# Kernel tuning notes

Measured on AMD Instinct MI355X. Metric: run time of the kernel, lower is better.

## Reference

```python
import jax, jax.numpy as jnp
import numpy as np


def setup_inputs() -> dict:
    key = jax.random.key(0)
    kx, ky = jax.random.split(key)
    B, N, M, D = 4, 4096, 4096, 128
    xd = jax.random.normal(kx, (B, N, D), dtype=jnp.float32)
    yd = jax.random.normal(ky, (B, M, D), dtype=jnp.float32)
    mask = jnp.ones((B, N, M), dtype=jnp.float32)
    return {"xd": xd, "yd": yd, "mask": mask}


def _pairwise_l2(x, y):
    # x: (B, N, D), y: (B, M, D) -> (B, N, M) euclidean distances
    x2 = jnp.sum(x * x, axis=-1)[:, :, None]          # (B, N, 1)
    y2 = jnp.sum(y * y, axis=-1)[:, None, :]          # (B, 1, M)
    xy = jnp.einsum("bnd,bmd->bnm", x, y)             # (B, N, M)
    d2 = jnp.maximum(x2 + y2 - 2.0 * xy, 0.0)
    return jnp.sqrt(d2)


def reference(xd, yd, mask):
    # NNDFMatcher.forward: orientation='x', smallest=True, topk=None
    dists = _pairwise_l2(xd, yd) * mask               # (B, N, M)
    pairs = jnp.argmin(dists, axis=-1)                # (B, N) int
    top_dists = jnp.min(dists, axis=-1)               # (B, N)
    M = mask.shape[-1]
    # one-hot scatter: match_mask[b, n, pairs[b, n]] = 1
    match_mask = (pairs[..., None] == jnp.arange(M)[None, None, :]).astype(mask.dtype)
    return match_mask, pairs, top_dists
```

## Files before the change

kernel.cpp:

```cpp
#include <hip/hip_runtime.h>


typedef float  f32x4  __attribute__((ext_vector_type(4)));
typedef short  bf16x8 __attribute__((ext_vector_type(8)));

#define PS ((size_t)2097152)

#define WAITVM_(N) asm volatile("s_waitcnt vmcnt(" #N ")" ::: "memory")
#define WAITVM(N)  WAITVM_(N)
#define BAR        __builtin_amdgcn_s_barrier()

__device__ __forceinline__ unsigned short f2bf(float x) {
    unsigned u = __float_as_uint(x);
    u += 0x7FFFu + ((u >> 16) & 1u);
    return (unsigned short)(u >> 16);
}
__device__ __forceinline__ float bf2f(unsigned short s) {
    return __uint_as_float(((unsigned)s) << 16);
}
__device__ __forceinline__ void gload_lds16(const void* g, void* l) {
    __builtin_amdgcn_global_load_lds(
        (const __attribute__((address_space(1))) void*)g,
        (__attribute__((address_space(3))) void*)l, 16, 0, 0);
}

__global__ __launch_bounds__(256) void k_prep(const float* __restrict__ xd,
                                              const float* __restrict__ yd,
                                              unsigned short* __restrict__ pl,
                                              float* __restrict__ ws) {
    __shared__ float sm[4][16];
    int bid  = blockIdx.x;
    int i    = bid >> 10;
    int b    = (bid >> 8) & 3;
    int rblk = bid & 255;
    int tid  = threadIdx.x;
    int kb   = tid >> 6;
    int l    = tid & 63;
    int r    = rblk * 16 + (l & 15);
    int k0   = kb * 32 + ((l >> 4) & 3) * 8;
    const float* src = (i ? yd : xd) + ((size_t)(b * 4096 + r) * 128 + k0);
    float v[8];
    *reinterpret_cast<float4*>(v)     = *reinterpret_cast<const float4*>(src);
    *reinterpret_cast<float4*>(v + 4) = *reinterpret_cast<const float4*>(src + 4);
    bf16x8 hv, mv, lv;
    float s = 0.f;
    #pragma unroll
    for (int e = 0; e < 8; ++e) {
        float x = v[e];
        s = fmaf(x, x, s);
        unsigned short h  = f2bf(x);
        float r1 = x - bf2f(h);
        unsigned short m  = f2bf(r1);
        float r2 = r1 - bf2f(m);
        unsigned short lo = f2bf(r2);
        hv[e] = (short)h; mv[e] = (short)m; lv[e] = (short)lo;
    }
    int rt = rblk >> 3, rb = rblk & 7, kh = kb >> 1, kc = kb & 1;
    size_t base = ((((size_t)((b * 2 + kh) * 32 + rt)) * 8 + rb) * 2 + kc) * 512 + (size_t)l * 8;
    unsigned short* dst = pl + (size_t)(i * 3) * PS;
    *reinterpret_cast<bf16x8*>(dst + base)          = hv;
    *reinterpret_cast<bf16x8*>(dst + base + PS)     = mv;
    *reinterpret_cast<bf16x8*>(dst + base + 2 * PS) = lv;
    s += __shfl_xor(s, 16);
    s += __shfl_xor(s, 32);
    if (l < 16) sm[kb][l] = s;
    __syncthreads();
    if (tid < 16) {
        float t = sm[0][tid] + sm[1][tid] + sm[2][tid] + sm[3][tid];
        ws[(i ? 16384 : 0) + b * 4096 + rblk * 16 + tid] = t;
    }
}

__global__ __launch_bounds__(512, 2) void k_gemm(const float* __restrict__ mask,
                                                 const float* __restrict__ ws,
                                                 const unsigned short* __restrict__ pl,
                                                 float* __restrict__ out,
                                                 float* __restrict__ pv,
                                                 int* __restrict__ pi) {
    __shared__ __align__(16) unsigned short Ab[2][3][8192];
    __shared__ __align__(16) unsigned short Bs[3][8192];
    __shared__ __align__(16) float y2s[2048];
    __shared__ float candv[128][4];
    __shared__ int   candi[128][4];

    const int bid = blockIdx.x;
    const int xcd = bid & 7;
    const int b   = xcd >> 1;
    const int ch  = xcd & 1;
    const int rt  = bid >> 3;
    const int tid = threadIdx.x;
    const int w   = tid >> 6, l = tid & 63;
    const int wr  = w >> 2, wc = w & 3;
    const int lg4 = (l >> 4) & 3, l15 = l & 15;
    const int g0  = b * 4096 + rt * 128;

    float x2r[16];
    #pragma unroll
    for (int mi = 0; mi < 4; ++mi)
        #pragma unroll
        for (int rg = 0; rg < 4; ++rg)
            x2r[mi * 4 + rg] = ws[g0 + wr * 64 + mi * 16 + lg4 * 4 + rg];

    #pragma unroll
    for (int c = 0; c < 6; ++c) {
        const int kh = c / 3, ap = c % 3;
        const unsigned short* Ac = pl + (size_t)ap * PS
            + (((size_t)((b * 2 + kh) * 32 + rt)) << 13);
        const char* g = (const char*)Ac + w * 1024 + l * 16;
        char* dd = (char*)(&Ab[kh][ap][0]) + w * 1024;
        gload_lds16(g, dd);
        gload_lds16(g + 8192, dd + 8192);
    }
    {
        const char* g = (const char*)(ws + 16384 + b * 4096 + ch * 2048) + w * 1024 + l * 16;
        gload_lds16(g, (char*)y2s + w * 1024);
    }

#define STAGE_B(NTT, CC, SLOT) do {                                               \
    const int kh_ = (CC) / 3, bp_ = (CC) % 3;                                     \
    const unsigned short* Bc_ = pl + (size_t)(3 + bp_) * PS                       \
        + (((size_t)((b * 2 + kh_) * 32 + (ch * 16 + (NTT)))) << 13);             \
    const char* g_ = (const char*)Bc_ + w * 1024 + l * 16;                        \
    char* d_ = (char*)(&Bs[SLOT][0]) + w * 1024;                                  \
    gload_lds16(g_, d_);                                                          \
    gload_lds16(g_ + 8192, d_ + 8192);                                            \
} while (0)

    STAGE_B(0, 0, 0);
    STAGE_B(0, 1, 1);
    WAITVM(2);
    BAR;

    float bv[16];
    int   bi[16];
    #pragma unroll
    for (int q = 0; q < 16; ++q) { bv[q] = 3.4e38f; bi[q] = 0; }

    f32x4 acc[4][2];
    float pm[32];

#define MLOAD(K) do {                                                             \
    const int mi_ = (K) >> 3, rg_ = ((K) >> 1) & 3, ni_ = (K) & 1;                \
    pm[K] = mask[(size_t)(g0 + wr * 64 + mi_ * 16 + lg4 * 4 + rg_) * 4096         \
                 + (ch * 2048 + nt * 128 + wc * 32 + ni_ * 16 + l15)];            \
} while (0)

#define ZST(I) do {                                                               \
    const f32x4 z_ = (f32x4){0.f, 0.f, 0.f, 0.f};                                 \
    const int r_ = (tid >> 5) * 8 + (I);                                          \
    *reinterpret_cast<f32x4*>(out + (size_t)(g0 + r_) * 4096                      \
        + ch * 2048 + nt * 128 + ((tid & 31) << 2)) = z_;                         \
} while (0)

#define COMPUTE(CC, SLOT) do {                                                    \
    const int kh_ = (CC) / 3, bp_ = (CC) % 3;                                     \
    const int lim_ = (bp_ == 0) ? 2 : (bp_ == 1) ? 1 : 0;                         \
    bf16x8 bfr_[2][2];                                                            \
    _Pragma("unroll") for (int ni = 0; ni < 2; ++ni)                              \
    _Pragma("unroll") for (int kc = 0; kc < 2; ++kc)                              \
        bfr_[ni][kc] = *reinterpret_cast<const bf16x8*>(                          \
            &Bs[SLOT][(((wc * 2 + ni) * 2 + kc) << 9) + l * 8]);                  \
    __builtin_amdgcn_s_setprio(1);                                                \
    _Pragma("unroll") for (int ap = 0; ap < 3; ++ap) {                            \
        if (ap <= lim_) {                                                         \
            _Pragma("unroll") for (int mi = 0; mi < 4; ++mi) {                    \
                _Pragma("unroll") for (int kc = 0; kc < 2; ++kc) {                \
                    bf16x8 af_ = *reinterpret_cast<const bf16x8*>(                \
                        &Ab[kh_][ap][(((wr * 4 + mi) * 2 + kc) << 9) + l * 8]);   \
                    _Pragma("unroll") for (int ni = 0; ni < 2; ++ni)              \
                        acc[mi][ni] = __builtin_amdgcn_mfma_f32_16x16x32_bf16(    \
                            af_, bfr_[ni][kc], acc[mi][ni], 0, 0, 0);             \
                }                                                                 \
            }                                                                     \
        }                                                                         \
    }                                                                             \
    __builtin_amdgcn_s_setprio(0);                                                \
} while (0)

    for (int nt = 0; nt < 16; ++nt) {
        const int ntn = (nt < 15) ? nt + 1 : 15;
        #pragma unroll
        for (int mi = 0; mi < 4; ++mi)
            #pragma unroll
            for (int ni = 0; ni < 2; ++ni) acc[mi][ni] = (f32x4){0.f, 0.f, 0.f, 0.f};

        STAGE_B(nt, 2, 2);
        MLOAD(0); MLOAD(1); MLOAD(2); MLOAD(3); MLOAD(4); MLOAD(5);
        ZST(0); ZST(1);
        COMPUTE(0, 0);
        WAITVM(10); BAR;
        STAGE_B(nt, 3, 0);
        MLOAD(6); MLOAD(7); MLOAD(8); MLOAD(9); MLOAD(10); MLOAD(11);
        ZST(2); ZST(3);
        COMPUTE(1, 1);
        WAITVM(18); BAR;
        STAGE_B(nt, 4, 1);
        MLOAD(12); MLOAD(13); MLOAD(14); MLOAD(15); MLOAD(16); MLOAD(17);
        ZST(4);
        COMPUTE(2, 2);
        WAITVM(17); BAR;
        STAGE_B(nt, 5, 2);
        MLOAD(18); MLOAD(19); MLOAD(20); MLOAD(21); MLOAD(22); MLOAD(23);
        ZST(5);
        COMPUTE(3, 0);
        WAITVM(16); BAR;
        STAGE_B(ntn, 0, 0);
        MLOAD(24); MLOAD(25); MLOAD(26); MLOAD(27);
        ZST(6);
        COMPUTE(4, 1);
        WAITVM(14); BAR;
        MLOAD(28); MLOAD(29); MLOAD(30); MLOAD(31);
        STAGE_B(ntn, 1, 1);
        ZST(7);
        COMPUTE(5, 2);
        WAITVM(12); BAR;

        WAITVM(3);
        #pragma unroll
        for (int ni = 0; ni < 2; ++ni) {
            const int c = ch * 2048 + nt * 128 + wc * 32 + ni * 16 + l15;
            float y2v = y2s[nt * 128 + wc * 32 + ni * 16 + l15];
            #pragma unroll
            for (int mi = 0; mi < 4; ++mi) {
                #pragma unroll
                for (int rg = 0; rg < 4; ++rg) {
                    float d2 = x2r[mi * 4 + rg] + y2v - 2.0f * acc[mi][ni][rg];
                    float d  = sqrtf(fmaxf(d2, 0.0f)) * pm[mi * 8 + rg * 2 + ni];
                    const int q = mi * 4 + rg;
                    if (d < bv[q]) { bv[q] = d; bi[q] = c; }
                }
            }
        }
    }
#undef STAGE_B
#undef MLOAD
#undef ZST
#undef COMPUTE

    #pragma unroll
    for (int off = 1; off < 16; off <<= 1) {
        #pragma unroll
        for (int q = 0; q < 16; ++q) {
            float ov = __shfl_xor(bv[q], off);
            int   oi = __shfl_xor(bi[q], off);
            if (ov < bv[q] || (ov == bv[q] && oi < bi[q])) { bv[q] = ov; bi[q] = oi; }
        }
    }
    if (l15 == 0) {
        #pragma unroll
        for (int mi = 0; mi < 4; ++mi)
            #pragma unroll
            for (int rg = 0; rg < 4; ++rg) {
                int rowl = wr * 64 + mi * 16 + lg4 * 4 + rg;
                candv[rowl][wc] = bv[mi * 4 + rg];
                candi[rowl][wc] = bi[mi * 4 + rg];
            }
    }
    __syncthreads();
    if (tid < 128) {
        float v  = candv[tid][0];
        int   ix = candi[tid][0];
        #pragma unroll
        for (int t = 1; t < 4; ++t) {
            float v2 = candv[tid][t];
            int   i2 = candi[tid][t];
            if (v2 < v || (v2 == v && i2 < ix)) { v = v2; ix = i2; }
        }
        int grow = g0 + tid;
        pv[grow * 2 + ch] = v;
        pi[grow * 2 + ch] = ix;
    }
}

__global__ __launch_bounds__(256) void k_fin(const float* __restrict__ pv,
                                             const int* __restrict__ pi,
                                             float* __restrict__ out) {
    int t = blockIdx.x * 256 + threadIdx.x;
    float v0 = pv[t * 2], v1 = pv[t * 2 + 1];
    int   i0 = pi[t * 2], i1 = pi[t * 2 + 1];
    bool take1 = (v1 < v0) || (v1 == v0 && i1 < i0);
    float v  = take1 ? v1 : v0;
    int   ix = take1 ? i1 : i0;
    out[67108864 + t]         = (float)ix;
    out[67108864 + 16384 + t] = v;
    out[(size_t)t * 4096 + (size_t)ix] = 1.0f;
}

__global__ __launch_bounds__(256) void k_rowsq(const float* __restrict__ xd,
                                               const float* __restrict__ yd,
                                               float* __restrict__ ws) {
    int tid  = threadIdx.x;
    int wid  = tid >> 6, lane = tid & 63;
    int gr   = blockIdx.x * 4 + wid;
    const float* src = (gr < 16384) ? (xd + (size_t)gr * 128)
                                    : (yd + (size_t)(gr - 16384) * 128);
    float2 v = reinterpret_cast<const float2*>(src)[lane];
    float s  = v.x * v.x + v.y * v.y;
    for (int off = 32; off > 0; off >>= 1) s += __shfl_down(s, off);
    if (lane == 0) ws[gr] = s;
}

__global__ __launch_bounds__(256, 1) void k_main_fb(const float* __restrict__ xd,
                                                    const float* __restrict__ yd,
                                                    const float* __restrict__ mask,
                                                    const float* __restrict__ ws,
                                                    float* __restrict__ pvals,
                                                    int* __restrict__ pidx,
                                                    float* __restrict__ mm) {
    __shared__ __align__(16) float Xs[128 * 128];
    __shared__ __align__(16) float Ys[128 * 128];
    const int bid  = blockIdx.x;
    const int mh   = bid & 1;
    const int rb   = (bid >> 1) & 31;
    const int b    = bid >> 6;
    const int tid  = threadIdx.x;
    const int ty   = tid >> 4;
    const int tx   = tid & 15;
    const int row0 = rb * 128;
    const int m0   = mh * 2048;
    {
        const float4 z = make_float4(0.f, 0.f, 0.f, 0.f);
        size_t base = ((size_t)(b * 4096 + row0)) * 4096 + (size_t)m0;
        for (int r = 0; r < 128; ++r) {
            float4* p = reinterpret_cast<float4*>(mm + base + (size_t)r * 4096);
            p[tid] = z; p[tid + 256] = z;
        }
    }
    {
        int lrow = tid >> 5, slot = tid & 31;
        for (int p = 0; p < 16; ++p) {
            int row  = p * 8 + lrow;
            float4 v = reinterpret_cast<const float4*>(
                           xd + ((size_t)(b * 4096 + row0 + row)) * 128)[slot];
            int ss = slot ^ (row & 31);
            *reinterpret_cast<float4*>(&Xs[row * 128 + (ss << 2)]) = v;
        }
    }
    float x2r[8];
    #pragma unroll
    for (int i = 0; i < 8; ++i) x2r[i] = ws[b * 4096 + row0 + ty * 8 + i];
    const float* y2g = ws + 16384 + b * 4096;
    float bv[8]; int bi[8];
    #pragma unroll
    for (int i = 0; i < 8; ++i) { bv[i] = 3.4e38f; bi[i] = 0; }
    __syncthreads();
    for (int tile = 0; tile < 16; ++tile) {
        const int mbase = m0 + tile * 128;
        {
            int lrow = tid >> 5, slot = tid & 31;
            for (int p = 0; p < 16; ++p) {
                int row  = p * 8 + lrow;
                float4 v = reinterpret_cast<const float4*>(
                               yd + ((size_t)(b * 4096 + mbase + row)) * 128)[slot];
                int ss = slot ^ (row & 31);
                *reinterpret_cast<float4*>(&Ys[row * 128 + (ss << 2)]) = v;
            }
        }
        __syncthreads();
        float acc[8][8];
        #pragma unroll
        for (int i = 0; i < 8; ++i)
            #pragma unroll
            for (int jj = 0; jj < 8; ++jj) acc[i][jj] = 0.0f;
        #pragma unroll 4
        for (int ks = 0; ks < 32; ++ks) {
            float4 bf[8];
            #pragma unroll
            for (int jj = 0; jj < 8; ++jj) {
                int c = jj * 16 + tx;
                bf[jj] = *reinterpret_cast<const float4*>(&Ys[c * 128 + ((ks ^ (c & 31)) << 2)]);
            }
            #pragma unroll
            for (int i = 0; i < 8; ++i) {
                int r = ty * 8 + i;
                float4 a = *reinterpret_cast<const float4*>(&Xs[r * 128 + ((ks ^ (r & 31)) << 2)]);
                #pragma unroll
                for (int jj = 0; jj < 8; ++jj) {
                    acc[i][jj] = fmaf(a.x, bf[jj].x, acc[i][jj]);
                    acc[i][jj] = fmaf(a.y, bf[jj].y, acc[i][jj]);
                    acc[i][jj] = fmaf(a.z, bf[jj].z, acc[i][jj]);
                    acc[i][jj] = fmaf(a.w, bf[jj].w, acc[i][jj]);
                }
            }
        }
        float y2v[8];
        #pragma unroll
        for (int jj = 0; jj < 8; ++jj) y2v[jj] = y2g[mbase + jj * 16 + tx];
        #pragma unroll
        for (int i = 0; i < 8; ++i) {
            int r = ty * 8 + i;
            const float* mr = mask + ((size_t)(b * 4096 + row0 + r)) * 4096;
            #pragma unroll
            for (int jj = 0; jj < 8; ++jj) {
                int   m  = mbase + jj * 16 + tx;
                float d2 = x2r[i] + y2v[jj] - 2.0f * acc[i][jj];
                float d  = sqrtf(fmaxf(d2, 0.0f)) * mr[m];
                if (d < bv[i]) { bv[i] = d; bi[i] = m; }
            }
        }
        __syncthreads();
    }
    float* candv = Xs;
    int*   candi = reinterpret_cast<int*>(Xs + 2048);
    #pragma unroll
    for (int i = 0; i < 8; ++i) {
        int r = ty * 8 + i;
        candv[r * 16 + tx] = bv[i];
        candi[r * 16 + tx] = bi[i];
    }
    __syncthreads();
    if (tid < 128) {
        int   r  = tid;
        float v  = candv[r * 16];
        int   ix = candi[r * 16];
        for (int t = 1; t < 16; ++t) {
            float v2 = candv[r * 16 + t];
            int   i2 = candi[r * 16 + t];
            if (v2 < v || (v2 == v && i2 < ix)) { v = v2; ix = i2; }
        }
        int grow = b * 4096 + row0 + r;
        pvals[grow * 2 + mh] = v;
        pidx [grow * 2 + mh] = ix;
    }
}

__global__ __launch_bounds__(256) void k_fin_fb(const float* __restrict__ pvals,
                                                const int* __restrict__ pidx,
                                                float* __restrict__ out) {
    int t = blockIdx.x * 256 + threadIdx.x;
    float v0 = pvals[t * 2], v1 = pvals[t * 2 + 1];
    int   i0 = pidx [t * 2], i1 = pidx [t * 2 + 1];
    bool take1 = (v1 < v0) || (v1 == v0 && i1 < i0);
    float v  = take1 ? v1 : v0;
    int   ix = take1 ? i1 : i0;
    out[67108864 + t]         = (float)ix;
    out[67108864 + 16384 + t] = v;
    out[(size_t)t * 4096 + (size_t)ix] = 1.0f;
}

extern "C" void kernel_launch(void* const* d_in, const int* in_sizes, int n_in,
                              void* d_out, int out_size, void* d_ws, size_t ws_size,
                              hipStream_t stream) {
    const float* xd   = (const float*)d_in[0];
    const float* yd   = (const float*)d_in[1];
    const float* mask = (const float*)d_in[2];
    float* out = (float*)d_out;
    float* wsf = (float*)d_ws;

    const size_t need = 131072 + 6 * PS * 2 + 262144;
    if (ws_size >= need) {
        unsigned short* pl = (unsigned short*)((char*)d_ws + 131072);
        float* pv = (float*)((char*)d_ws + 131072 + 6 * PS * 2);
        int*   pi = (int*)  ((char*)d_ws + 131072 + 6 * PS * 2 + 131072);
        k_prep <<<2048, 256, 0, stream>>>(xd, yd, pl, wsf);
        k_gemm <<<256,  512, 0, stream>>>(mask, wsf, pl, out, pv, pi);
        k_fin  <<<64,   256, 0, stream>>>(pv, pi, out);
    } else {
        float* pvals = wsf + 32768;
        int*   pidx  = (int*)(wsf + 65536);
        k_rowsq  <<<8192, 256, 0, stream>>>(xd, yd, wsf);
        k_main_fb<<<256,  256, 0, stream>>>(xd, yd, mask, wsf, pvals, pidx, out);
        k_fin_fb <<<64,   256, 0, stream>>>(pvals, pidx, out);
    }
}
```

Baseline: 202.1 us.

## Halve GEMM block tile and stream B fragments through registers instead of LDS

The fused distance/argmin GEMM kernel moves from 512-thread blocks covering 128 rows to 256-thread blocks covering 64 rows, and launches twice as many blocks. B operand fragments are now read straight from global memory into double-buffered registers, one k-chunk ahead, instead of being staged in an LDS ring. This removes the per-chunk barriers and vmcnt bookkeeping, and all mask loads are issued up front each column tile. In exchange each B tile is fetched by twice as many blocks, adding L2/global traffic. Global-load latency is also less hidden, because vmcnt waits for the register prefetch are in-order with the mask loads and zero-stores.

```diff
diff --git a/kernel.cpp b/kernel.cpp
--- a/kernel.cpp
+++ b/kernel.cpp
@@ -6,9 +6,8 @@
 
 #define PS ((size_t)2097152)
 
-#define WAITVM_(N) asm volatile("s_waitcnt vmcnt(" #N ")" ::: "memory")
-#define WAITVM(N)  WAITVM_(N)
-#define BAR        __builtin_amdgcn_s_barrier()
+#define WAITVM0 asm volatile("s_waitcnt vmcnt(0)" ::: "memory")
+#define BAR     __builtin_amdgcn_s_barrier()
 
 __device__ __forceinline__ unsigned short f2bf(float x) {
     unsigned u = __float_as_uint(x);
@@ -71,17 +70,16 @@
     }
 }
 
-__global__ __launch_bounds__(512, 2) void k_gemm(const float* __restrict__ mask,
+__global__ __launch_bounds__(256, 2) void k_gemm(const float* __restrict__ mask,
                                                  const float* __restrict__ ws,
                                                  const unsigned short* __restrict__ pl,
                                                  float* __restrict__ out,
                                                  float* __restrict__ pv,
                                                  int* __restrict__ pi) {
-    __shared__ __align__(16) unsigned short Ab[2][3][8192];
-    __shared__ __align__(16) unsigned short Bs[3][8192];
+    __shared__ __align__(16) unsigned short Ab[2][3][4096];
     __shared__ __align__(16) float y2s[2048];
-    __shared__ float candv[128][4];
-    __shared__ int   candi[128][4];
+    __shared__ float candv[64][4];
+    __shared__ int   candi[64][4];
 
     const int bid = blockIdx.x;
     const int xcd = bid & 7;
@@ -90,45 +88,47 @@
     const int rt  = bid >> 3;
     const int tid = threadIdx.x;
     const int w   = tid >> 6, l = tid & 63;
-    const int wr  = w >> 2, wc = w & 3;
+    const int wc  = w;
     const int lg4 = (l >> 4) & 3, l15 = l & 15;
-    const int g0  = b * 4096 + rt * 128;
+    const int g0  = b * 4096 + rt * 64;
 
     float x2r[16];
     #pragma unroll
     for (int mi = 0; mi < 4; ++mi)
         #pragma unroll
         for (int rg = 0; rg < 4; ++rg)
-            x2r[mi * 4 + rg] = ws[g0 + wr * 64 + mi * 16 + lg4 * 4 + rg];
+            x2r[mi * 4 + rg] = ws[g0 + mi * 16 + lg4 * 4 + rg];
 
     #pragma unroll
     for (int c = 0; c < 6; ++c) {
         const int kh = c / 3, ap = c % 3;
         const unsigned short* Ac = pl + (size_t)ap * PS
-            + (((size_t)((b * 2 + kh) * 32 + rt)) << 13);
+            + (((size_t)((b * 2 + kh) * 32 + (rt >> 1))) << 13) + ((size_t)(rt & 1) << 12);
         const char* g = (const char*)Ac + w * 1024 + l * 16;
         char* dd = (char*)(&Ab[kh][ap][0]) + w * 1024;
         gload_lds16(g, dd);
-        gload_lds16(g + 8192, dd + 8192);
+        gload_lds16(g + 4096, dd + 4096);
     }
     {
         const char* g = (const char*)(ws + 16384 + b * 4096 + ch * 2048) + w * 1024 + l * 16;
         gload_lds16(g, (char*)y2s + w * 1024);
-    }
-
-#define STAGE_B(NTT, CC, SLOT) do {                                               \
+        gload_lds16(g + 4096, (char*)y2s + w * 1024 + 4096);
+    }
+
+    bf16x8 Breg0[4], Breg1[4];
+
+#define PREFB(DST, NTT, CC) do {                                                  \
     const int kh_ = (CC) / 3, bp_ = (CC) % 3;                                     \
     const unsigned short* Bc_ = pl + (size_t)(3 + bp_) * PS                       \
-        + (((size_t)((b * 2 + kh_) * 32 + (ch * 16 + (NTT)))) << 13);             \
-    const char* g_ = (const char*)Bc_ + w * 1024 + l * 16;                        \
-    char* d_ = (char*)(&Bs[SLOT][0]) + w * 1024;                                  \
-    gload_lds16(g_, d_);                                                          \
-    gload_lds16(g_ + 8192, d_ + 8192);                                            \
+        + (((size_t)((b * 2 + kh_) * 32 + ch * 16 + (NTT))) << 13);               \
+    _Pragma("unroll") for (int ni = 0; ni < 2; ++ni)                              \
+    _Pragma("unroll") for (int kc = 0; kc < 2; ++kc)                              \
+        DST[ni * 2 + kc] = *reinterpret_cast<const bf16x8*>(                      \
+            Bc_ + (((wc * 2 + ni) * 2 + kc) << 9) + l * 8);                       \
 } while (0)
 
-    STAGE_B(0, 0, 0);
-    STAGE_B(0, 1, 1);
-    WAITVM(2);
+    PREFB(Breg0, 0, 0);
+    WAITVM0;
     BAR;
 
     float bv[16];
@@ -141,7 +141,7 @@
 
 #define MLOAD(K) do {                                                             \
     const int mi_ = (K) >> 3, rg_ = ((K) >> 1) & 3, ni_ = (K) & 1;                \
-    pm[K] = mask[(size_t)(g0 + wr * 64 + mi_ * 16 + lg4 * 4 + rg_) * 4096         \
+    pm[K] = mask[(size_t)(g0 + mi_ * 16 + lg4 * 4 + rg_) * 4096                   \
                  + (ch * 2048 + nt * 128 + wc * 32 + ni_ * 16 + l15)];            \
 } while (0)
 
@@ -152,24 +152,19 @@
         + ch * 2048 + nt * 128 + ((tid & 31) << 2)) = z_;                         \
 } while (0)
 
-#define COMPUTE(CC, SLOT) do {                                                    \
+#define COMPUTE(CC, BREG) do {                                                    \
     const int kh_ = (CC) / 3, bp_ = (CC) % 3;                                     \
     const int lim_ = (bp_ == 0) ? 2 : (bp_ == 1) ? 1 : 0;                         \
-    bf16x8 bfr_[2][2];                                                            \
-    _Pragma("unroll") for (int ni = 0; ni < 2; ++ni)                              \
-    _Pragma("unroll") for (int kc = 0; kc < 2; ++kc)                              \
-        bfr_[ni][kc] = *reinterpret_cast<const bf16x8*>(                          \
-            &Bs[SLOT][(((wc * 2 + ni) * 2 + kc) << 9) + l * 8]);                  \
     __builtin_amdgcn_s_setprio(1);                                                \
     _Pragma("unroll") for (int ap = 0; ap < 3; ++ap) {                            \
         if (ap <= lim_) {                                                         \
             _Pragma("unroll") for (int mi = 0; mi < 4; ++mi) {                    \
                 _Pragma("unroll") for (int kc = 0; kc < 2; ++kc) {                \
                     bf16x8 af_ = *reinterpret_cast<const bf16x8*>(                \
-                        &Ab[kh_][ap][(((wr * 4 + mi) * 2 + kc) << 9) + l * 8]);   \
+                        &Ab[kh_][ap][((mi * 2 + kc) << 9) + l * 8]);              \
                     _Pragma("unroll") for (int ni = 0; ni < 2; ++ni)              \
                         acc[mi][ni] = __builtin_amdgcn_mfma_f32_16x16x32_bf16(    \
-                            af_, bfr_[ni][kc], acc[mi][ni], 0, 0, 0);             \
+                            af_, BREG[ni * 2 + kc], acc[mi][ni], 0, 0, 0);        \
                 }                                                                 \
             }                                                                     \
         }                                                                         \
@@ -177,6 +172,7 @@
     __builtin_amdgcn_s_setprio(0);                                                \
 } while (0)
 
+    #pragma unroll 1
     for (int nt = 0; nt < 16; ++nt) {
         const int ntn = (nt < 15) ? nt + 1 : 15;
         #pragma unroll
@@ -184,38 +180,20 @@
             #pragma unroll
             for (int ni = 0; ni < 2; ++ni) acc[mi][ni] = (f32x4){0.f, 0.f, 0.f, 0.f};
 
-        STAGE_B(nt, 2, 2);
-        MLOAD(0); MLOAD(1); MLOAD(2); MLOAD(3); MLOAD(4); MLOAD(5);
-        ZST(0); ZST(1);
-        COMPUTE(0, 0);
-        WAITVM(10); BAR;
-        STAGE_B(nt, 3, 0);
-        MLOAD(6); MLOAD(7); MLOAD(8); MLOAD(9); MLOAD(10); MLOAD(11);
-        ZST(2); ZST(3);
-        COMPUTE(1, 1);
-        WAITVM(18); BAR;
-        STAGE_B(nt, 4, 1);
+        MLOAD(0);  MLOAD(1);  MLOAD(2);  MLOAD(3);  MLOAD(4);  MLOAD(5);
+        MLOAD(6);  MLOAD(7);  MLOAD(8);  MLOAD(9);  MLOAD(10); MLOAD(11);
         MLOAD(12); MLOAD(13); MLOAD(14); MLOAD(15); MLOAD(16); MLOAD(17);
-        ZST(4);
-        COMPUTE(2, 2);
-        WAITVM(17); BAR;
-        STAGE_B(nt, 5, 2);
         MLOAD(18); MLOAD(19); MLOAD(20); MLOAD(21); MLOAD(22); MLOAD(23);
-        ZST(5);
-        COMPUTE(3, 0);
-        WAITVM(16); BAR;
-        STAGE_B(ntn, 0, 0);
-        MLOAD(24); MLOAD(25); MLOAD(26); MLOAD(27);
-        ZST(6);
-        COMPUTE(4, 1);
-        WAITVM(14); BAR;
-        MLOAD(28); MLOAD(29); MLOAD(30); MLOAD(31);
-        STAGE_B(ntn, 1, 1);
-        ZST(7);
-        COMPUTE(5, 2);
-        WAITVM(12); BAR;
-
-        WAITVM(3);
+        MLOAD(24); MLOAD(25); MLOAD(26); MLOAD(27); MLOAD(28); MLOAD(29);
+        MLOAD(30); MLOAD(31);
+
+        PREFB(Breg1, nt, 1);  ZST(0); ZST(1);  COMPUTE(0, Breg0);
+        PREFB(Breg0, nt, 2);  ZST(2); ZST(3);  COMPUTE(1, Breg1);
+        PREFB(Breg1, nt, 3);  ZST(4);          COMPUTE(2, Breg0);
+        PREFB(Breg0, nt, 4);  ZST(5);          COMPUTE(3, Breg1);
+        PREFB(Breg1, nt, 5);  ZST(6);          COMPUTE(4, Breg0);
+        PREFB(Breg0, ntn, 0); ZST(7);          COMPUTE(5, Breg1);
+
         #pragma unroll
         for (int ni = 0; ni < 2; ++ni) {
             const int c = ch * 2048 + nt * 128 + wc * 32 + ni * 16 + l15;
@@ -232,7 +210,7 @@
             }
         }
     }
-#undef STAGE_B
+#undef PREFB
 #undef MLOAD
 #undef ZST
 #undef COMPUTE
@@ -251,13 +229,13 @@
         for (int mi = 0; mi < 4; ++mi)
             #pragma unroll
             for (int rg = 0; rg < 4; ++rg) {
-                int rowl = wr * 64 + mi * 16 + lg4 * 4 + rg;
+                int rowl = mi * 16 + lg4 * 4 + rg;
                 candv[rowl][wc] = bv[mi * 4 + rg];
                 candi[rowl][wc] = bi[mi * 4 + rg];
             }
     }
     __syncthreads();
-    if (tid < 128) {
+    if (tid < 64) {
         float v  = candv[tid][0];
         int   ix = candi[tid][0];
         #pragma unroll
@@ -453,7 +431,7 @@
         float* pv = (float*)((char*)d_ws + 131072 + 6 * PS * 2);
         int*   pi = (int*)  ((char*)d_ws + 131072 + 6 * PS * 2 + 131072);
         k_prep <<<2048, 256, 0, stream>>>(xd, yd, pl, wsf);
-        k_gemm <<<256,  512, 0, stream>>>(mask, wsf, pl, out, pv, pi);
+        k_gemm <<<512,  256, 0, stream>>>(mask, wsf, pl, out, pv, pi);
         k_fin  <<<64,   256, 0, stream>>>(pv, pi, out);
     } else {
         float* pvals = wsf + 32768;
```

After: 408.9 us. 102% more time.
